# Kernel tuning notes

Hardware: AMD Instinct MI355X
Metric: run time of the kernel (lower is better)

## Reference

```python
import jax, jax.numpy as jnp
import numpy as np

N, E, D, H = 100000, 20000, 64, 4
NNZ = 500000
NEG_SLOPE_ATT = 0.2   # PyG HypergraphConv attention leaky_relu slope
NEG_SLOPE_FFN = 0.01  # nn.LeakyReLU default
LN_EPS = 1e-5


def setup_inputs() -> dict:
    key = jax.random.key(0)
    ks = jax.random.split(key, 10)
    s = 0.05
    return {
        "x": jax.random.normal(ks[0], (N, D), jnp.float32),
        "adj_row": jax.random.randint(ks[1], (NNZ,), 0, N),
        "adj_col": jax.random.randint(ks[2], (NNZ,), 0, E),
        "adj_val": jax.random.uniform(ks[3], (NNZ,), jnp.float32) + 0.1,
        "num_edges": E,
        "lin_w": jax.random.normal(ks[4], (H * D, D), jnp.float32) * s,
        "att": jax.random.normal(ks[5], (1, H, 2 * D), jnp.float32) * s,
        "bias": jnp.zeros((D,), jnp.float32),
        "ln1_g": jnp.ones((D,), jnp.float32),
        "ln1_b": jnp.zeros((D,), jnp.float32),
        "ln2_g": jnp.ones((D,), jnp.float32),
        "ln2_b": jnp.zeros((D,), jnp.float32),
        "w1": jax.random.normal(ks[6], (D, D), jnp.float32) * s,
        "b1": jnp.zeros((D,), jnp.float32),
        "w2": jax.random.normal(ks[7], (D, D), jnp.float32) * s,
        "b2": jnp.zeros((D,), jnp.float32),
    }


def _layer_norm(x, g, b):
    mu = jnp.mean(x, axis=-1, keepdims=True)
    var = jnp.mean((x - mu) ** 2, axis=-1, keepdims=True)
    return (x - mu) * jax.lax.rsqrt(var + LN_EPS) * g + b


def _hypergraph_layer(x, adj_row, adj_col, adj_val, num_edges,
                      lin_w, att, bias, ln1_g, ln1_b, ln2_g, ln2_b,
                      w1, b1, w2, b2):
    n = x.shape[0]
    # --- get_hyperedge_representation: omega = diag(1/colsum) @ H^T @ x ---
    colsum = jax.ops.segment_sum(adj_val, adj_col, num_segments=num_edges)  # [E]
    omega = jax.ops.segment_sum(adj_val[:, None] * x[adj_row], adj_col,
                                num_segments=num_edges) / colsum[:, None]  # [E, D]
    # --- HypergraphConv (use_attention=True, concat=False) ---
    xh = (x @ lin_w.T).reshape(n, H, D)              # [N, H, D]
    eh = (omega @ lin_w.T).reshape(num_edges, H, D)  # [E, H, D]
    att_x, att_e = att[0, :, :D], att[0, :, D:]      # [H, D] each
    s_n = jnp.einsum('nhd,hd->nh', xh, att_x)        # [N, H]
    s_e = jnp.einsum('ehd,hd->eh', eh, att_e)        # [E, H]
    alpha = jax.nn.leaky_relu(s_n[adj_row] + s_e[adj_col], NEG_SLOPE_ATT)  # [NNZ, H]
    # softmax over incidences grouped by hyperedge (attention_mode='node')
    amax = jax.ops.segment_max(alpha, adj_col, num_segments=num_edges)
    ea = jnp.exp(alpha - amax[adj_col])
    alpha = ea / jax.ops.segment_sum(ea, adj_col, num_segments=num_edges)[adj_col]
    # degree normalizations D (node) and B (hyperedge)
    d_deg = jax.ops.segment_sum(adj_val[adj_col], adj_row, num_segments=n)
    d_inv = jnp.where(d_deg > 0, 1.0 / d_deg, 0.0)
    b_deg = jax.ops.segment_sum(jnp.ones_like(adj_val), adj_col, num_segments=num_edges)
    b_inv = jnp.where(b_deg > 0, 1.0 / b_deg, 0.0)
    # pass 1: nodes -> hyperedges  (norm_i = B at target edge)
    msg1 = b_inv[adj_col][:, None, None] * xh[adj_row] * alpha[:, :, None]
    edge_out = jax.ops.segment_sum(msg1, adj_col, num_segments=num_edges)  # [E,H,D]
    # pass 2: hyperedges -> nodes  (norm_i = D at target node)
    msg2 = d_inv[adj_row][:, None, None] * edge_out[adj_col] * alpha[:, :, None]
    node_out = jax.ops.segment_sum(msg2, adj_row, num_segments=n)  # [N,H,D]
    conv = jnp.mean(node_out, axis=1) + bias  # concat=False -> head mean
    # --- residual + norm + FFN (Linear, Linear, LeakyReLU) ---
    h = _layer_norm(x + conv, ln1_g, ln1_b)
    ffn = jax.nn.leaky_relu((h @ w1.T + b1) @ w2.T + b2, NEG_SLOPE_FFN)
    return _layer_norm(h + ffn, ln2_g, ln2_b)


def reference(x, adj_row, adj_col, adj_val, num_edges, lin_w, att, bias,
              ln1_g, ln1_b, ln2_g, ln2_b, w1, b1, w2, b2):
    return _hypergraph_layer(x, adj_row, adj_col, adj_val, num_edges,
                             lin_w, att, bias, ln1_g, ln1_b, ln2_g, ln2_b,
                             w1, b1, w2, b2)
```

## Files before the change

kernel.cpp:

```cpp
#include <hip/hip_runtime.h>

#define N_NODES 100000
#define N_EDGES 20000
#define DIM 64
#define HEADS 4
#define NNZ_ 500000
#define LNEPS 1e-5f

__device__ __forceinline__ float wsum64(float v){
#pragma unroll
  for (int off = 32; off; off >>= 1) v += __shfl_xor(v, off);
  return v;
}
__device__ __forceinline__ float wmax64(float v){
#pragma unroll
  for (int off = 32; off; off >>= 1) v = fmaxf(v, __shfl_xor(v, off));
  return v;
}
__device__ __forceinline__ float lrelu2(float a){ return a > 0.f ? a : 0.2f*a; }

__device__ __forceinline__ unsigned bfpack(float a, float b){
  unsigned ua = __float_as_uint(a), ub = __float_as_uint(b);
  ua += 0x7fffu + ((ua >> 16) & 1u);
  ub += 0x7fffu + ((ub >> 16) & 1u);
  return (ua >> 16) | (ub & 0xffff0000u);
}
__device__ __forceinline__ unsigned short bf16of(float f){
  unsigned u = __float_as_uint(f);
  u += 0x7fffu + ((u >> 16) & 1u);
  return (unsigned short)(u >> 16);
}
__device__ __forceinline__ float bfup(unsigned short s){
  return __uint_as_float(((unsigned)s) << 16);
}

__global__ __launch_bounds__(256) void k_hist(const int* __restrict__ row,
                                              const int* __restrict__ col,
                                              const float* __restrict__ val,
                                              int* __restrict__ ecnt, int* __restrict__ ncnt,
                                              float* __restrict__ colsum, float* __restrict__ ddeg){
  int i = blockIdx.x*256 + threadIdx.x;
  if (i >= NNZ_) return;
  int c = col[i], r = row[i];
  atomicAdd(&ecnt[c], 1);
  atomicAdd(&ncnt[r], 1);
  atomicAdd(&colsum[c], val[i]);
  atomicAdd(&ddeg[r], val[c]);
}

__device__ __forceinline__ void scanA_body(const int* cnt, int* ptr, int* bsum,
                                           int n, int blk){
  __shared__ int wsums[16];
  int idx = blk*1024 + threadIdx.x;
  int lane = threadIdx.x & 63, wid = threadIdx.x >> 6;
  int v = (idx < n) ? cnt[idx] : 0;
  int s = v;
#pragma unroll
  for (int off = 1; off < 64; off <<= 1){
    int t = __shfl_up(s, off);
    if (lane >= off) s += t;
  }
  if (lane == 63) wsums[wid] = s;
  __syncthreads();
  if (wid == 0 && lane < 16){
    int ws = wsums[lane];
    int t = ws;
#pragma unroll
    for (int off = 1; off < 16; off <<= 1){
      int u = __shfl_up(t, off);
      if (lane >= off) t += u;
    }
    wsums[lane] = t - ws;
  }
  __syncthreads();
  if (idx < n) ptr[idx] = wsums[wid] + s - v;
  if (threadIdx.x == 1023) bsum[blk] = wsums[15] + s;
}

__global__ __launch_bounds__(1024) void k_scanA2(const int* __restrict__ ecnt,
                                                 int* __restrict__ colptr,
                                                 int* __restrict__ bsumE, int nbE,
                                                 const int* __restrict__ ncnt,
                                                 int* __restrict__ rowptr,
                                                 int* __restrict__ bsumN){
  int b = blockIdx.x;
  if (b < nbE) scanA_body(ecnt, colptr, bsumE, N_EDGES, b);
  else         scanA_body(ncnt, rowptr, bsumN, N_NODES, b - nbE);
}

__device__ __forceinline__ void scanB_body(int* bsum, int nb, int* ptr, int n){
  __shared__ int sh[256];
  int t = threadIdx.x;
  int v = (t < nb) ? bsum[t] : 0;
  sh[t] = v;
  __syncthreads();
  for (int off = 1; off < 256; off <<= 1){
    int u = (t >= off) ? sh[t-off] : 0;
    __syncthreads();
    sh[t] += u;
    __syncthreads();
  }
  if (t < nb) bsum[t] = sh[t] - v;
  if (t == nb-1) ptr[n] = sh[t];
}

__global__ __launch_bounds__(256) void k_scanB2(int* __restrict__ bsumE, int nbE,
                                                int* __restrict__ colptr,
                                                int* __restrict__ bsumN, int nbN,
                                                int* __restrict__ rowptr){
  if (blockIdx.x == 0) scanB_body(bsumE, nbE, colptr, N_EDGES);
  else                 scanB_body(bsumN, nbN, rowptr, N_NODES);
}

__global__ __launch_bounds__(1024) void k_scanC2(int* __restrict__ colptr,
                                                 const int* __restrict__ bsumE, int nbE,
                                                 int* __restrict__ rowptr,
                                                 const int* __restrict__ bsumN){
  int b = blockIdx.x;
  if (b < nbE){
    int idx = b*1024 + threadIdx.x;
    if (idx < N_EDGES) colptr[idx] += bsumE[b];
  } else {
    int idx = (b - nbE)*1024 + threadIdx.x;
    if (idx < N_NODES) rowptr[idx] += bsumN[b - nbE];
  }
}

__global__ __launch_bounds__(256) void k_scatter(const int* __restrict__ row,
                                                 const int* __restrict__ col,
                                                 const float* __restrict__ val,
                                                 const int* __restrict__ colptr,
                                                 const int* __restrict__ rowptr,
                                                 int* __restrict__ ecur, int* __restrict__ ncur,
                                                 int4* __restrict__ rvp){
  int i = blockIdx.x*256 + threadIdx.x;
  if (i >= NNZ_) return;
  int c = col[i], r = row[i];
  int p = atomicAdd(&ecur[c], 1);
  int q = atomicAdd(&ncur[r], 1);
  rvp[colptr[c] + p] = make_int4(r, __float_as_int(val[i]), rowptr[r] + q, 0);
}

__global__ __launch_bounds__(256) void k_watt(const float* __restrict__ lin_w,
                                              const float* __restrict__ att,
                                              float* __restrict__ wattx,
                                              float* __restrict__ watte){
  int j = threadIdx.x;
  int h = j >> 6;
  float sx = 0.f, se = 0.f;
#pragma unroll
  for (int d = 0; d < DIM; ++d){
    float w = lin_w[(h*DIM + d)*DIM + (j & 63)];
    sx = fmaf(att[h*2*DIM + d],       w, sx);
    se = fmaf(att[h*2*DIM + DIM + d], w, se);
  }
  wattx[j] = sx;
  watte[j] = se;
}

__global__ __launch_bounds__(256) void k_wfold(const float* __restrict__ w1,
                                               const float* __restrict__ w2,
                                               const float* __restrict__ b1,
                                               const float* __restrict__ b2,
                                               float* __restrict__ Wf,
                                               float* __restrict__ bp){
  int tid = threadIdx.x;
#pragma unroll
  for (int m = 0; m < 16; ++m){
    int idx = m*256 + tid;
    int o = idx >> 6, k = idx & 63;
    float s = 0.f;
#pragma unroll
    for (int i = 0; i < 64; ++i)
      s = fmaf(w2[o*64 + i], w1[i*64 + k], s);
    Wf[idx] = s;
  }
  if (tid < 64){
    float s = b2[tid];
#pragma unroll
    for (int i = 0; i < 64; ++i)
      s = fmaf(w2[tid*64 + i], b1[i], s);
    bp[tid] = s;
  }
}

__global__ __launch_bounds__(128) void k_pre(const float* __restrict__ x,
                                             const float* __restrict__ wattx,
                                             const float* __restrict__ watte,
                                             float4* __restrict__ snpe,
                                             unsigned short* __restrict__ xb){
  int lane = threadIdx.x & 63, wid = threadIdx.x >> 6;
  int n = blockIdx.x*2 + wid;
  if (n >= N_NODES) return;
  float xv = x[(size_t)n*DIM + lane];
  xb[(size_t)n*DIM + lane] = bf16of(xv);
  float s0 = wsum64(xv*wattx[lane]);
  float s1 = wsum64(xv*wattx[64+lane]);
  float s2 = wsum64(xv*wattx[128+lane]);
  float s3 = wsum64(xv*wattx[192+lane]);
  float p0 = wsum64(xv*watte[lane]);
  float p1 = wsum64(xv*watte[64+lane]);
  float p2 = wsum64(xv*watte[128+lane]);
  float p3 = wsum64(xv*watte[192+lane]);
  if (lane == 0){
    snpe[2*(size_t)n    ] = make_float4(s0,s1,s2,s3);
    snpe[2*(size_t)n + 1] = make_float4(p0,p1,p2,p3);
  }
}

__global__ __launch_bounds__(128) void k_softagg(const int* __restrict__ colptr,
                                                 const int4* __restrict__ rvp,
                                                 const float4* __restrict__ snpe,
                                                 const float* __restrict__ colsum,
                                                 const unsigned short* __restrict__ xb,
                                                 float4* __restrict__ alphaC,
                                                 int4* __restrict__ cealpha,
                                                 unsigned short* __restrict__ aggB){
  __shared__ float4 aSh[128];
  int lane = threadIdx.x & 63, wid = threadIdx.x >> 6;
  int e = blockIdx.x*2 + wid;
  if (e >= N_EDGES) return;
  int sb = __builtin_amdgcn_readfirstlane(colptr[e]);
  int cnt = __builtin_amdgcn_readfirstlane(colptr[e+1]) - sb;
  if (cnt == 0) return;
  float rcs = 1.0f / colsum[e];
  float acc0=0,acc1=0,acc2=0,acc3=0;

  if (cnt <= 64){
    bool act = lane < cnt;
    int r = 0, rp = 0; float v = 0.f;
    float4 snv = make_float4(0,0,0,0), p = make_float4(0,0,0,0);
    if (act){
      int4 m = rvp[sb+lane];
      r = m.x; v = __int_as_float(m.y); rp = m.z;
      snv = snpe[2*(size_t)r];
      p   = snpe[2*(size_t)r + 1];
    }
    float se0 = wsum64(v*p.x)*rcs, se1 = wsum64(v*p.y)*rcs,
          se2 = wsum64(v*p.z)*rcs, se3 = wsum64(v*p.w)*rcs;
    float t0 = act ? lrelu2(snv.x+se0) : -1e30f;
    float t1 = act ? lrelu2(snv.y+se1) : -1e30f;
    float t2 = act ? lrelu2(snv.z+se2) : -1e30f;
    float t3 = act ? lrelu2(snv.w+se3) : -1e30f;
    float m0 = wmax64(t0), m1 = wmax64(t1), m2 = wmax64(t2), m3 = wmax64(t3);
    float e0 = act ? __expf(t0-m0) : 0.f;
    float e1 = act ? __expf(t1-m1) : 0.f;
    float e2 = act ? __expf(t2-m2) : 0.f;
    float e3 = act ? __expf(t3-m3) : 0.f;
    float q0 = wsum64(e0), q1 = wsum64(e1), q2 = wsum64(e2), q3 = wsum64(e3);
    float4 a = make_float4(e0/q0, e1/q1, e2/q2, e3/q3);
    if (act)
      cealpha[rp] = make_int4(e, (int)bfpack(a.x,a.y), (int)bfpack(a.z,a.w), 0);
    aSh[wid*64 + lane] = a;

    int k = 0;
    for (; k + 4 <= cnt; k += 4){
      int r0 = rvp[sb+k].x, r1 = rvp[sb+k+1].x, r2 = rvp[sb+k+2].x, r3 = rvp[sb+k+3].x;
      float4 a0 = aSh[wid*64+k], a1 = aSh[wid*64+k+1],
             a2 = aSh[wid*64+k+2], a3 = aSh[wid*64+k+3];
      float x0 = bfup(xb[(size_t)r0*DIM + lane]);
      float x1 = bfup(xb[(size_t)r1*DIM + lane]);
      float x2 = bfup(xb[(size_t)r2*DIM + lane]);
      float x3 = bfup(xb[(size_t)r3*DIM + lane]);
      acc0 = fmaf(a0.x, x0, acc0); acc1 = fmaf(a0.y, x0, acc1);
      acc2 = fmaf(a0.z, x0, acc2); acc3 = fmaf(a0.w, x0, acc3);
      acc0 = fmaf(a1.x, x1, acc0); acc1 = fmaf(a1.y, x1, acc1);
      acc2 = fmaf(a1.z, x1, acc2); acc3 = fmaf(a1.w, x1, acc3);
      acc0 = fmaf(a2.x, x2, acc0); acc1 = fmaf(a2.y, x2, acc1);
      acc2 = fmaf(a2.z, x2, acc2); acc3 = fmaf(a2.w, x2, acc3);
      acc0 = fmaf(a3.x, x3, acc0); acc1 = fmaf(a3.y, x3, acc1);
      acc2 = fmaf(a3.z, x3, acc2); acc3 = fmaf(a3.w, x3, acc3);
    }
    for (; k < cnt; ++k){
      int r0 = rvp[sb+k].x;
      float4 a0 = aSh[wid*64+k];
      float x0 = bfup(xb[(size_t)r0*DIM + lane]);
      acc0 = fmaf(a0.x, x0, acc0); acc1 = fmaf(a0.y, x0, acc1);
      acc2 = fmaf(a0.z, x0, acc2); acc3 = fmaf(a0.w, x0, acc3);
    }
  } else {
    int s = sb;
    float a0=0,a1=0,a2=0,a3=0;
    for (int base = 0; base < cnt; base += 64){
      int j = s + base + lane;
      if (base + lane < cnt){
        int4 m = rvp[j];
        float v = __int_as_float(m.y);
        float4 p = snpe[2*(size_t)m.x + 1];
        a0 = fmaf(v,p.x,a0); a1 = fmaf(v,p.y,a1); a2 = fmaf(v,p.z,a2); a3 = fmaf(v,p.w,a3);
      }
    }
    float se0 = wsum64(a0)*rcs, se1 = wsum64(a1)*rcs, se2 = wsum64(a2)*rcs, se3 = wsum64(a3)*rcs;
    float m0=-1e30f,m1=-1e30f,m2=-1e30f,m3=-1e30f;
    for (int base = 0; base < cnt; base += 64){
      int j = s + base + lane;
      if (base + lane < cnt){
        float4 snv = snpe[2*(size_t)rvp[j].x];
        m0 = fmaxf(m0, lrelu2(snv.x+se0)); m1 = fmaxf(m1, lrelu2(snv.y+se1));
        m2 = fmaxf(m2, lrelu2(snv.z+se2)); m3 = fmaxf(m3, lrelu2(snv.w+se3));
      }
    }
    m0 = wmax64(m0); m1 = wmax64(m1); m2 = wmax64(m2); m3 = wmax64(m3);
    float q0=0,q1=0,q2=0,q3=0;
    for (int base = 0; base < cnt; base += 64){
      int j = s + base + lane;
      if (base + lane < cnt){
        float4 snv = snpe[2*(size_t)rvp[j].x];
        float e0 = __expf(lrelu2(snv.x+se0)-m0), e1 = __expf(lrelu2(snv.y+se1)-m1);
        float e2 = __expf(lrelu2(snv.z+se2)-m2), e3 = __expf(lrelu2(snv.w+se3)-m3);
        q0+=e0; q1+=e1; q2+=e2; q3+=e3;
        alphaC[j] = make_float4(e0,e1,e2,e3);
      }
    }
    q0 = wsum64(q0); q1 = wsum64(q1); q2 = wsum64(q2); q3 = wsum64(q3);
    float r0 = 1.f/q0, r1 = 1.f/q1, r2 = 1.f/q2, r3 = 1.f/q3;
    for (int base = 0; base < cnt; base += 64){
      int j = s + base + lane;
      if (base + lane < cnt){
        float4 av = alphaC[j];
        av = make_float4(av.x*r0, av.y*r1, av.z*r2, av.w*r3);
        alphaC[j] = av;
        cealpha[rvp[j].z] = make_int4(e, (int)bfpack(av.x,av.y), (int)bfpack(av.z,av.w), 0);
      }
    }
    for (int k = 0; k < cnt; ++k){
      int rj = rvp[sb+k].x;
      float4 al = alphaC[sb+k];
      float xv = bfup(xb[(size_t)rj*DIM + lane]);
      acc0 = fmaf(al.x, xv, acc0); acc1 = fmaf(al.y, xv, acc1);
      acc2 = fmaf(al.z, xv, acc2); acc3 = fmaf(al.w, xv, acc3);
    }
  }

  float binv = 1.0f/(float)cnt;
  size_t b = (size_t)e*256;
  aggB[b       + lane] = bf16of(acc0*binv);
  aggB[b +  64 + lane] = bf16of(acc1*binv);
  aggB[b + 128 + lane] = bf16of(acc2*binv);
  aggB[b + 192 + lane] = bf16of(acc3*binv);
}

__global__ __launch_bounds__(256) void k_eoT(const unsigned short* __restrict__ aggB,
                                             const float* __restrict__ lin_w,
                                             unsigned short* __restrict__ eoTb){
  __shared__ float L[16*260];
  int lane = threadIdx.x & 63, h = threadIdx.x >> 6;
  float w[64];
  const float4* wr = (const float4*)(lin_w + ((size_t)h*64 + lane)*64);
#pragma unroll
  for (int k = 0; k < 16; ++k){
    float4 t = wr[k];
    w[4*k] = t.x; w[4*k+1] = t.y; w[4*k+2] = t.z; w[4*k+3] = t.w;
  }
  int e0 = blockIdx.x*16;
#pragma unroll
  for (int el = 0; el < 16; el += 4){
    float av0 = bfup(aggB[(size_t)(e0+el  )*256 + h*64 + lane]);
    float av1 = bfup(aggB[(size_t)(e0+el+1)*256 + h*64 + lane]);
    float av2 = bfup(aggB[(size_t)(e0+el+2)*256 + h*64 + lane]);
    float av3 = bfup(aggB[(size_t)(e0+el+3)*256 + h*64 + lane]);
    float o0=0.f, o1=0.f, o2=0.f, o3=0.f;
#pragma unroll
    for (int k = 0; k < 64; ++k){
      float wk = w[k];
      o0 = fmaf(__shfl(av0, k), wk, o0);
      o1 = fmaf(__shfl(av1, k), wk, o1);
      o2 = fmaf(__shfl(av2, k), wk, o2);
      o3 = fmaf(__shfl(av3, k), wk, o3);
    }
    L[(el  )*260 + lane*4 + h] = o0;
    L[(el+1)*260 + lane*4 + h] = o1;
    L[(el+2)*260 + lane*4 + h] = o2;
    L[(el+3)*260 + lane*4 + h] = o3;
  }
  __syncthreads();
  int tid = threadIdx.x;
#pragma unroll
  for (int p = 0; p < 4; ++p){
    int el = p*4 + (tid >> 6);
    int l = tid & 63;
    const float* Lr = &L[el*260 + l*4];
    uint2 v;
    v.x = bfpack(Lr[0], Lr[1]);
    v.y = bfpack(Lr[2], Lr[3]);
    *(uint2*)(eoTb + (size_t)(e0+el)*256 + l*4) = v;
  }
}

#define ACC4(J, V, M) { \
  float u0 = __uint_as_float((V).x << 16); \
  float u1 = __uint_as_float((V).x & 0xffff0000u); \
  float u2 = __uint_as_float((V).y << 16); \
  float u3 = __uint_as_float((V).y & 0xffff0000u); \
  float ax = __uint_as_float(((unsigned)(M).y) << 16); \
  float ay = __uint_as_float(((unsigned)(M).y) & 0xffff0000u); \
  float az = __uint_as_float(((unsigned)(M).z) << 16); \
  float aw = __uint_as_float(((unsigned)(M).z) & 0xffff0000u); \
  acc[J][0] = fmaf(u0, ax, acc[J][0]); \
  acc[J][1] = fmaf(u1, ay, acc[J][1]); \
  acc[J][2] = fmaf(u2, az, acc[J][2]); \
  acc[J][3] = fmaf(u3, aw, acc[J][3]); }

#define SEG(J, KB, KE) do { \
    int k = (KB); \
    for (; k + 4 <= (KE); k += 4){ \
      int4 m0 = cealpha[k], m1 = cealpha[k+1], m2 = cealpha[k+2], m3 = cealpha[k+3]; \
      uint2 v0 = *(const uint2*)(eoTb + (size_t)m0.x*256 + lane*4); \
      uint2 v1 = *(const uint2*)(eoTb + (size_t)m1.x*256 + lane*4); \
      uint2 v2 = *(const uint2*)(eoTb + (size_t)m2.x*256 + lane*4); \
      uint2 v3 = *(const uint2*)(eoTb + (size_t)m3.x*256 + lane*4); \
      ACC4(J, v0, m0); ACC4(J, v1, m1); ACC4(J, v2, m2); ACC4(J, v3, m3); \
    } \
    for (; k < (KE); ++k){ \
      int4 m0 = cealpha[k]; \
      uint2 v0 = *(const uint2*)(eoTb + (size_t)m0.x*256 + lane*4); \
      ACC4(J, v0, m0); \
    } \
  } while(0)

__global__ __launch_bounds__(128) void k_final2(const float* __restrict__ x,
                                                const int* __restrict__ rowptr,
                                                const int4* __restrict__ cealpha,
                                                const unsigned short* __restrict__ eoTb,
                                                const float* __restrict__ ddeg,
                                                const float* __restrict__ bias,
                                                const float* __restrict__ g1,
                                                const float* __restrict__ b1g,
                                                const float* __restrict__ g2,
                                                const float* __restrict__ b2g,
                                                const float* __restrict__ Wf,
                                                const float* __restrict__ bp,
                                                float* __restrict__ out){
  int lane = threadIdx.x & 63, wid = threadIdx.x >> 6;
  int nbase = blockIdx.x*8 + wid*4;
  int q0 = __builtin_amdgcn_readfirstlane(rowptr[nbase]);
  int q1 = __builtin_amdgcn_readfirstlane(rowptr[nbase+1]);
  int q2 = __builtin_amdgcn_readfirstlane(rowptr[nbase+2]);
  int q3 = __builtin_amdgcn_readfirstlane(rowptr[nbase+3]);
  int q4 = __builtin_amdgcn_readfirstlane(rowptr[nbase+4]);

  float xv[4];
#pragma unroll
  for (int j = 0; j < 4; ++j) xv[j] = x[(size_t)(nbase+j)*DIM + lane];
  float dd0 = ddeg[nbase], dd1 = ddeg[nbase+1], dd2 = ddeg[nbase+2], dd3 = ddeg[nbase+3];

  float acc[4][4];
#pragma unroll
  for (int j = 0; j < 4; ++j)
#pragma unroll
    for (int h = 0; h < 4; ++h) acc[j][h] = 0.f;

  SEG(0, q0, q1);
  SEG(1, q1, q2);
  SEG(2, q2, q3);
  SEG(3, q3, q4);

  float w[64];
  const float4* wr = (const float4*)(Wf + (size_t)lane*64);
#pragma unroll
  for (int k = 0; k < 16; ++k){
    float4 t = wr[k];
    w[4*k] = t.x; w[4*k+1] = t.y; w[4*k+2] = t.z; w[4*k+3] = t.w;
  }
  float biasv = bias[lane], bpv = bp[lane];
  float g1v = g1[lane], b1gv = b1g[lane], g2v = g2[lane], b2gv = b2g[lane];

  float ddv[4] = {dd0, dd1, dd2, dd3};
  float hs[4];
#pragma unroll
  for (int j = 0; j < 4; ++j){
    float dd = ddv[j];
    float dinv = dd > 0.f ? 0.25f/dd : 0.f;
    float conv = (acc[j][0]+acc[j][1]+acc[j][2]+acc[j][3])*dinv;
    float t = xv[j] + conv + biasv;
    float mu = wsum64(t) * (1.f/64.f);
    float dv = t - mu;
    float var = wsum64(dv*dv) * (1.f/64.f);
    hs[j] = dv * rsqrtf(var + LNEPS) * g1v + b1gv;
  }

  float a0 = bpv, a1 = bpv, a2 = bpv, a3 = bpv;
#pragma unroll
  for (int k = 0; k < 64; ++k){
    a0 = fmaf(__shfl(hs[0], k), w[k], a0);
    a1 = fmaf(__shfl(hs[1], k), w[k], a1);
    a2 = fmaf(__shfl(hs[2], k), w[k], a2);
    a3 = fmaf(__shfl(hs[3], k), w[k], a3);
  }

  float fa[4] = {a0, a1, a2, a3};
#pragma unroll
  for (int j = 0; j < 4; ++j){
    int n = nbase + j;
    float ffn = fa[j] > 0.f ? fa[j] : 0.01f*fa[j];
    float t2 = hs[j] + ffn;
    float mu2 = wsum64(t2) * (1.f/64.f);
    float dv2 = t2 - mu2;
    float var2 = wsum64(dv2*dv2) * (1.f/64.f);
    out[(size_t)n*DIM + lane] = dv2 * rsqrtf(var2 + LNEPS) * g2v + b2gv;
  }
}

extern "C" void kernel_launch(void* const* d_in, const int* in_sizes, int n_in,
                              void* d_out, int out_size, void* d_ws, size_t ws_size,
                              hipStream_t stream){
  const float* x     = (const float*)d_in[0];
  const int*   row   = (const int*)d_in[1];
  const int*   col   = (const int*)d_in[2];
  const float* val   = (const float*)d_in[3];
  const float* lin_w = (const float*)d_in[5];
  const float* att   = (const float*)d_in[6];
  const float* bias  = (const float*)d_in[7];
  const float* g1    = (const float*)d_in[8];
  const float* b1g   = (const float*)d_in[9];
  const float* g2    = (const float*)d_in[10];
  const float* b2g   = (const float*)d_in[11];
  const float* w1    = (const float*)d_in[12];
  const float* b1    = (const float*)d_in[13];
  const float* w2    = (const float*)d_in[14];
  const float* b2    = (const float*)d_in[15];
  float* out = (float*)d_out;
  float* ws  = (float*)d_ws;

  constexpr size_t E = N_EDGES, Nn = N_NODES;
  constexpr size_t o_ecnt   = 0;
  constexpr size_t o_ncnt   = o_ecnt + E;
  constexpr size_t o_ecur   = o_ncnt + Nn;
  constexpr size_t o_ncur   = o_ecur + E;
  constexpr size_t o_colsum = o_ncur + Nn;
  constexpr size_t o_ddeg   = o_colsum + E;
  constexpr size_t ZEND     = o_ddeg + Nn;
  constexpr size_t o_colptr = ZEND;
  constexpr size_t o_rowptr = o_colptr + E + 4;
  constexpr size_t o_bsumE  = o_rowptr + Nn + 4;
  constexpr size_t o_bsumN  = o_bsumE + 256;
  constexpr size_t o_rvp    = (o_bsumN + 256 + 3) & ~(size_t)3;
  constexpr size_t o_wattx  = o_rvp + 4*(size_t)NNZ_;
  constexpr size_t o_watte  = o_wattx + 256;
  constexpr size_t o_Wf     = o_watte + 256;
  constexpr size_t o_bp     = o_Wf + 4096;
  constexpr size_t o_snpe   = o_bp + 64;
  constexpr size_t o_alphaC = o_snpe + 8*Nn;
  constexpr size_t o_ceal   = o_alphaC + 4*(size_t)NNZ_;
  constexpr size_t o_xb     = o_ceal + 4*(size_t)NNZ_;
  constexpr size_t o_aggB   = o_xb + 32*Nn;
  constexpr size_t o_eo     = o_aggB + 128*E;

  int*    ecnt   = (int*)(ws + o_ecnt);
  int*    ncnt   = (int*)(ws + o_ncnt);
  int*    ecur   = (int*)(ws + o_ecur);
  int*    ncur   = (int*)(ws + o_ncur);
  float*  colsum = ws + o_colsum;
  float*  ddeg   = ws + o_ddeg;
  int*    colptr = (int*)(ws + o_colptr);
  int*    rowptr = (int*)(ws + o_rowptr);
  int*    bsumE  = (int*)(ws + o_bsumE);
  int*    bsumN  = (int*)(ws + o_bsumN);
  int4*   rvp    = (int4*)(ws + o_rvp);
  float*  wattx  = ws + o_wattx;
  float*  watte  = ws + o_watte;
  float*  Wf     = ws + o_Wf;
  float*  bp     = ws + o_bp;
  float4* snpe   = (float4*)(ws + o_snpe);
  float4* alphaC = (float4*)(ws + o_alphaC);
  int4*   cealpha= (int4*)(ws + o_ceal);
  unsigned short* xb   = (unsigned short*)(ws + o_xb);
  unsigned short* aggB = (unsigned short*)(ws + o_aggB);
  unsigned short* eoTb = (unsigned short*)(ws + o_eo);

  hipMemsetAsync(ws, 0, ZEND*sizeof(float), stream);

  k_hist<<<(NNZ_+255)/256, 256, 0, stream>>>(row, col, val, ecnt, ncnt, colsum, ddeg);

  int nbE = (int)((E + 1023)/1024);
  int nbN = (int)((Nn + 1023)/1024);
  k_scanA2<<<nbE + nbN, 1024, 0, stream>>>(ecnt, colptr, bsumE, nbE, ncnt, rowptr, bsumN);
  k_scanB2<<<2, 256, 0, stream>>>(bsumE, nbE, colptr, bsumN, nbN, rowptr);
  k_scanC2<<<nbE + nbN, 1024, 0, stream>>>(colptr, bsumE, nbE, rowptr, bsumN);

  k_scatter<<<(NNZ_+255)/256, 256, 0, stream>>>(row, col, val, colptr, rowptr,
                                                ecur, ncur, rvp);

  k_watt<<<1, 256, 0, stream>>>(lin_w, att, wattx, watte);
  k_wfold<<<1, 256, 0, stream>>>(w1, w2, b1, b2, Wf, bp);
  k_pre<<<(int)((Nn+1)/2), 128, 0, stream>>>(x, wattx, watte, snpe, xb);
  k_softagg<<<(int)((E+1)/2), 128, 0, stream>>>(colptr, rvp, snpe, colsum, xb,
                                                alphaC, cealpha, aggB);
  k_eoT<<<(int)(E/16), 256, 0, stream>>>(aggB, lin_w, eoTb);
  k_final2<<<(int)(Nn/8), 128, 0, stream>>>(x, rowptr, cealpha, eoTb, ddeg,
                                            bias, g1, b1g, g2, b2g, Wf, bp, out);
}
```

Before: 449.6 us.

## Store edge outputs as per-head planes and gather head-by-head in final kernel

Edge outputs are now written as four separate head planes of 64 bf16 values per edge, not as an interleaved 256-wide row. This drops the shared-memory transpose and its barrier in k_eoT. k_final2 loops over heads, gathering a 2-byte value per lane from one plane at a time, so each head's working set is a quarter of the edge table and may fit cache better. The cost is four passes over the cealpha index list, narrower gathers per request, and less per-load parallelism.

```diff
diff --git a/kernel.cpp b/kernel.cpp
--- a/kernel.cpp
+++ b/kernel.cpp
@@ -32,6 +32,10 @@
 }
 __device__ __forceinline__ float bfup(unsigned short s){
   return __uint_as_float(((unsigned)s) << 16);
+}
+__device__ __forceinline__ float alphaOf(const int4& m, int H){
+  unsigned u = (H < 2) ? (unsigned)m.y : (unsigned)m.z;
+  return __uint_as_float((H & 1) ? (u & 0xffff0000u) : (u << 16));
 }
 
 __global__ __launch_bounds__(256) void k_hist(const int* __restrict__ row,
@@ -342,8 +346,7 @@
 
 __global__ __launch_bounds__(256) void k_eoT(const unsigned short* __restrict__ aggB,
                                              const float* __restrict__ lin_w,
-                                             unsigned short* __restrict__ eoTb){
-  __shared__ float L[16*260];
+                                             unsigned short* __restrict__ eoP){
   int lane = threadIdx.x & 63, h = threadIdx.x >> 6;
   float w[64];
   const float4* wr = (const float4*)(lin_w + ((size_t)h*64 + lane)*64);
@@ -352,6 +355,7 @@
     float4 t = wr[k];
     w[4*k] = t.x; w[4*k+1] = t.y; w[4*k+2] = t.z; w[4*k+3] = t.w;
   }
+  unsigned short* plane = eoP + (size_t)h*N_EDGES*64;
   int e0 = blockIdx.x*16;
 #pragma unroll
   for (int el = 0; el < 16; el += 4){
@@ -368,60 +372,40 @@
       o2 = fmaf(__shfl(av2, k), wk, o2);
       o3 = fmaf(__shfl(av3, k), wk, o3);
     }
-    L[(el  )*260 + lane*4 + h] = o0;
-    L[(el+1)*260 + lane*4 + h] = o1;
-    L[(el+2)*260 + lane*4 + h] = o2;
-    L[(el+3)*260 + lane*4 + h] = o3;
-  }
-  __syncthreads();
-  int tid = threadIdx.x;
-#pragma unroll
-  for (int p = 0; p < 4; ++p){
-    int el = p*4 + (tid >> 6);
-    int l = tid & 63;
-    const float* Lr = &L[el*260 + l*4];
-    uint2 v;
-    v.x = bfpack(Lr[0], Lr[1]);
-    v.y = bfpack(Lr[2], Lr[3]);
-    *(uint2*)(eoTb + (size_t)(e0+el)*256 + l*4) = v;
-  }
-}
-
-#define ACC4(J, V, M) { \
-  float u0 = __uint_as_float((V).x << 16); \
-  float u1 = __uint_as_float((V).x & 0xffff0000u); \
-  float u2 = __uint_as_float((V).y << 16); \
-  float u3 = __uint_as_float((V).y & 0xffff0000u); \
-  float ax = __uint_as_float(((unsigned)(M).y) << 16); \
-  float ay = __uint_as_float(((unsigned)(M).y) & 0xffff0000u); \
-  float az = __uint_as_float(((unsigned)(M).z) << 16); \
-  float aw = __uint_as_float(((unsigned)(M).z) & 0xffff0000u); \
-  acc[J][0] = fmaf(u0, ax, acc[J][0]); \
-  acc[J][1] = fmaf(u1, ay, acc[J][1]); \
-  acc[J][2] = fmaf(u2, az, acc[J][2]); \
-  acc[J][3] = fmaf(u3, aw, acc[J][3]); }
-
-#define SEG(J, KB, KE) do { \
+    plane[(size_t)(e0+el  )*64 + lane] = bf16of(o0);
+    plane[(size_t)(e0+el+1)*64 + lane] = bf16of(o1);
+    plane[(size_t)(e0+el+2)*64 + lane] = bf16of(o2);
+    plane[(size_t)(e0+el+3)*64 + lane] = bf16of(o3);
+  }
+}
+
+#define SEGH(J, KB, KE, H, PL) do { \
     int k = (KB); \
     for (; k + 4 <= (KE); k += 4){ \
       int4 m0 = cealpha[k], m1 = cealpha[k+1], m2 = cealpha[k+2], m3 = cealpha[k+3]; \
-      uint2 v0 = *(const uint2*)(eoTb + (size_t)m0.x*256 + lane*4); \
-      uint2 v1 = *(const uint2*)(eoTb + (size_t)m1.x*256 + lane*4); \
-      uint2 v2 = *(const uint2*)(eoTb + (size_t)m2.x*256 + lane*4); \
-      uint2 v3 = *(const uint2*)(eoTb + (size_t)m3.x*256 + lane*4); \
-      ACC4(J, v0, m0); ACC4(J, v1, m1); ACC4(J, v2, m2); ACC4(J, v3, m3); \
+      float b0 = alphaOf(m0, H), b1 = alphaOf(m1, H), \
+            b2 = alphaOf(m2, H), b3 = alphaOf(m3, H); \
+      float v0 = bfup((PL)[(size_t)m0.x*64 + lane]); \
+      float v1 = bfup((PL)[(size_t)m1.x*64 + lane]); \
+      float v2 = bfup((PL)[(size_t)m2.x*64 + lane]); \
+      float v3 = bfup((PL)[(size_t)m3.x*64 + lane]); \
+      acc[J][H] = fmaf(v0, b0, acc[J][H]); \
+      acc[J][H] = fmaf(v1, b1, acc[J][H]); \
+      acc[J][H] = fmaf(v2, b2, acc[J][H]); \
+      acc[J][H] = fmaf(v3, b3, acc[J][H]); \
     } \
     for (; k < (KE); ++k){ \
       int4 m0 = cealpha[k]; \
-      uint2 v0 = *(const uint2*)(eoTb + (size_t)m0.x*256 + lane*4); \
-      ACC4(J, v0, m0); \
+      float b0 = alphaOf(m0, H); \
+      float v0 = bfup((PL)[(size_t)m0.x*64 + lane]); \
+      acc[J][H] = fmaf(v0, b0, acc[J][H]); \
     } \
   } while(0)
 
 __global__ __launch_bounds__(128) void k_final2(const float* __restrict__ x,
                                                 const int* __restrict__ rowptr,
                                                 const int4* __restrict__ cealpha,
-                                                const unsigned short* __restrict__ eoTb,
+                                                const unsigned short* __restrict__ eoP,
                                                 const float* __restrict__ ddeg,
                                                 const float* __restrict__ bias,
                                                 const float* __restrict__ g1,
@@ -450,10 +434,14 @@
 #pragma unroll
     for (int h = 0; h < 4; ++h) acc[j][h] = 0.f;
 
-  SEG(0, q0, q1);
-  SEG(1, q1, q2);
-  SEG(2, q2, q3);
-  SEG(3, q3, q4);
+#pragma unroll
+  for (int H = 0; H < 4; ++H){
+    const unsigned short* pl = eoP + (size_t)H*N_EDGES*64;
+    SEGH(0, q0, q1, H, pl);
+    SEGH(1, q1, q2, H, pl);
+    SEGH(2, q2, q3, H, pl);
+    SEGH(3, q3, q4, H, pl);
+  }
 
   float w[64];
   const float4* wr = (const float4*)(Wf + (size_t)lane*64);
@@ -566,7 +554,7 @@
   int4*   cealpha= (int4*)(ws + o_ceal);
   unsigned short* xb   = (unsigned short*)(ws + o_xb);
   unsigned short* aggB = (unsigned short*)(ws + o_aggB);
-  unsigned short* eoTb = (unsigned short*)(ws + o_eo);
+  unsigned short* eoP  = (unsigned short*)(ws + o_eo);
 
   hipMemsetAsync(ws, 0, ZEND*sizeof(float), stream);
 
@@ -586,7 +574,7 @@
   k_pre<<<(int)((Nn+1)/2), 128, 0, stream>>>(x, wattx, watte, snpe, xb);
   k_softagg<<<(int)((E+1)/2), 128, 0, stream>>>(colptr, rvp, snpe, colsum, xb,
                                                 alphaC, cealpha, aggB);
-  k_eoT<<<(int)(E/16), 256, 0, stream>>>(aggB, lin_w, eoTb);
-  k_final2<<<(int)(Nn/8), 128, 0, stream>>>(x, rowptr, cealpha, eoTb, ddeg,
+  k_eoT<<<(int)(E/16), 256, 0, stream>>>(aggB, lin_w, eoP);
+  k_final2<<<(int)(Nn/8), 128, 0, stream>>>(x, rowptr, cealpha, eoP, ddeg,
                                             bias, g1, b1g, g2, b2g, Wf, bp, out);
 }
```

New measurement: 455.6 us. About the same (+1.3%).
